# Kernel optimization log

Measured on AMD Instinct MI355X. Metric: run time of the kernel, lower is better.

Reference implementation:

```python
import jax, jax.numpy as jnp
import numpy as np

N, S, T, E, H = 4, 2048, 2048, 512, 8
HD = E // H  # head_dim = 64


def setup_inputs() -> dict:
    key0 = jax.random.key(0)
    ks = jax.random.split(key0, 12)
    sc = 1.0 / np.sqrt(E)
    inp = {
        "query": jax.random.normal(ks[0], (N, S, E), jnp.float32),
        "key": jax.random.normal(ks[1], (N, T, E), jnp.float32),
        "value": jax.random.normal(ks[2], (N, T, E), jnp.float32),
        "attn_mask": jnp.tril(jnp.ones((S, T), jnp.int32)),  # causal: 0 => masked
        # nn.Linear weights (out, in) and biases, torch convention y = x @ W.T + b
        "Wq": jax.random.normal(ks[3], (E, E), jnp.float32) * sc,
        "bq": jax.random.normal(ks[4], (E,), jnp.float32) * sc,
        "Wk": jax.random.normal(ks[5], (E, E), jnp.float32) * sc,
        "bk": jax.random.normal(ks[6], (E,), jnp.float32) * sc,
        "Wv": jax.random.normal(ks[7], (E, E), jnp.float32) * sc,
        "bv": jax.random.normal(ks[8], (E,), jnp.float32) * sc,
        "Wp": jax.random.normal(ks[9], (E, E), jnp.float32) * sc,
        "bp": jax.random.normal(ks[10], (E,), jnp.float32) * sc,
    }
    return inp


def reference(query, key, value, attn_mask, Wq, bq, Wk, bk, Wv, bv, Wp, bp):
    # QKV projections, split heads: (N, H, L, HD)
    q = (query @ Wq.T + bq).reshape(N, S, H, HD).transpose(0, 2, 1, 3)
    k = (key @ Wk.T + bk).reshape(N, T, H, HD).transpose(0, 2, 1, 3)
    v = (value @ Wv.T + bv).reshape(N, T, H, HD).transpose(0, 2, 1, 3)
    # scaled scores (N, H, S, T) -- intentionally materialized like the original
    e = jnp.einsum("nhsd,nhtd->nhst", q, k) / jnp.sqrt(jnp.float32(HD))
    e = jnp.where(attn_mask == 0, -jnp.inf, e)
    a = jax.nn.softmax(e, axis=-1)
    # dropout is identity in eval mode (reference runs deterministic/eval)
    y = jnp.einsum("nhst,nhtd->nhsd", a, v)
    y = y.transpose(0, 2, 1, 3).reshape(N, S, E)
    return y @ Wp.T + bp
```

## Files before the change

kernel.cpp:

```cpp
#include <hip/hip_runtime.h>


#define DEV __device__ __forceinline__

typedef unsigned short u16;
typedef unsigned int u32;
typedef __bf16 bf16x8 __attribute__((ext_vector_type(8)));
typedef float f32x4 __attribute__((ext_vector_type(4)));

#define MFMA_BF16(A, B, C) __builtin_amdgcn_mfma_f32_16x16x32_bf16(A, B, C, 0, 0, 0)

DEV u16 f2bf(float f) {
  u32 u = __builtin_bit_cast(u32, f);
  u += 0x7fffu + ((u >> 16) & 1u);
  return (u16)(u >> 16);
}
DEV u16 f2bf_ru(float f) {
  u32 u = __builtin_bit_cast(u32, f);
  return (u16)((u + 0x8000u) >> 16);
}

DEV void cp16(void* l, const void* g) {
  __builtin_amdgcn_global_load_lds(
      (const __attribute__((address_space(1))) u32*)g,
      (__attribute__((address_space(3))) u32*)l, 16, 0, 0);
}

__global__ __launch_bounds__(256) void cast3(const float* __restrict__ q,
                                             const float* __restrict__ k,
                                             const float* __restrict__ v,
                                             u16* qo, u16* ko, u16* vo) {
  const float* s = (blockIdx.y == 0) ? q : (blockIdx.y == 1) ? k : v;
  u16* d = (blockIdx.y == 0) ? qo : (blockIdx.y == 1) ? ko : vo;
  int i = blockIdx.x * 256 + threadIdx.x;
  float4 f = ((const float4*)s)[i];
  ushort4 o;
  o.x = f2bf(f.x); o.y = f2bf(f.y); o.z = f2bf(f.z); o.w = f2bf(f.w);
  ((ushort4*)d)[i] = o;
}

__global__ __launch_bounds__(256) void cast4(const float* __restrict__ a,
                                             const float* __restrict__ b,
                                             const float* __restrict__ c,
                                             const float* __restrict__ d2,
                                             u16* ao, u16* bo, u16* co, u16* do_) {
  int y = blockIdx.y;
  const float* s = (y == 0) ? a : (y == 1) ? b : (y == 2) ? c : d2;
  u16* d = (y == 0) ? ao : (y == 1) ? bo : (y == 2) ? co : do_;
  int i = blockIdx.x * 256 + threadIdx.x;
  float4 f = ((const float4*)s)[i];
  ushort4 o;
  o.x = f2bf(f.x); o.y = f2bf(f.y); o.z = f2bf(f.z); o.w = f2bf(f.w);
  ((ushort4*)d)[i] = o;
}

DEV void gemm_loop(const u16* __restrict__ A, const u16* __restrict__ W,
                   u16* As, u16* Bs, int m0, int n0, int tid, f32x4 acc[4][4]) {
  const int lane = tid & 63, wid = tid >> 6;
  const int wm = wid & 1, wn = wid >> 1;
  const int l15 = lane & 15, l4 = lane >> 4;
  for (int kt = 0; kt < 512; kt += 32) {
    __syncthreads();
#pragma unroll
    for (int i = 0; i < 2; ++i) {
      int c = tid + 256 * i;
      int row = c >> 2, kc = (c & 3) * 8;
      cp16(&As[c * 8], A + (m0 + row) * 512 + kt + kc);
      cp16(&Bs[c * 8], W + (n0 + row) * 512 + kt + kc);
    }
    __syncthreads();
    bf16x8 af[4], bfr[4];
#pragma unroll
    for (int f = 0; f < 4; ++f) {
      af[f]  = *(const bf16x8*)&As[(wm * 64 + f * 16 + l15) * 32 + l4 * 8];
      bfr[f] = *(const bf16x8*)&Bs[(wn * 64 + f * 16 + l15) * 32 + l4 * 8];
    }
#pragma unroll
    for (int fm = 0; fm < 4; ++fm)
#pragma unroll
      for (int fn = 0; fn < 4; ++fn)
        acc[fm][fn] = MFMA_BF16(af[fm], bfr[fn], acc[fm][fn]);
  }
}

__global__ __launch_bounds__(256) void gemm_qkv(
    const u16* __restrict__ qx, const u16* __restrict__ kx, const u16* __restrict__ vx,
    const u16* __restrict__ wq, const u16* __restrict__ wk, const u16* __restrict__ wv,
    const float* __restrict__ bq, const float* __restrict__ bk, const float* __restrict__ bv,
    u16* qp, u16* kp, u16* vp) {
  __shared__ u16 As[128 * 32];
  __shared__ u16 Bs[128 * 32];
  const int wsel = blockIdx.x >> 2;
  const u16* A = (wsel == 0) ? qx : (wsel == 1) ? kx : vx;
  const u16* W = (wsel == 0) ? wq : (wsel == 1) ? wk : wv;
  const float* bias = (wsel == 0) ? bq : (wsel == 1) ? bk : bv;
  u16* C = (wsel == 0) ? qp : (wsel == 1) ? kp : vp;
  const int n0 = (blockIdx.x & 3) * 128, m0 = blockIdx.y * 128;
  const int tid = threadIdx.x, lane = tid & 63, wid = tid >> 6;
  const int wm = wid & 1, wn = wid >> 1;
  const int l15 = lane & 15, l4 = lane >> 4;

  f32x4 acc[4][4] = {};
  gemm_loop(A, W, As, Bs, m0, n0, tid, acc);

#pragma unroll
  for (int fn = 0; fn < 4; ++fn) {
    int col = n0 + wn * 64 + fn * 16 + l15;
    float bvv = bias[col];
#pragma unroll
    for (int fm = 0; fm < 4; ++fm) {
      int rowb = m0 + wm * 64 + fm * 16 + l4 * 4;
#pragma unroll
      for (int r = 0; r < 4; ++r)
        C[(rowb + r) * 512 + col] = f2bf(acc[fm][fn][r] + bvv);
    }
  }
}

__global__ __launch_bounds__(256) void gemm_out(const u16* __restrict__ A,
                                                const u16* __restrict__ W,
                                                const float* __restrict__ bias,
                                                float* __restrict__ C) {
  __shared__ u16 As[128 * 32];
  __shared__ u16 Bs[128 * 32];
  const int n0 = blockIdx.x * 128, m0 = blockIdx.y * 128;
  const int tid = threadIdx.x, lane = tid & 63, wid = tid >> 6;
  const int wm = wid & 1, wn = wid >> 1;
  const int l15 = lane & 15, l4 = lane >> 4;

  f32x4 acc[4][4] = {};
  gemm_loop(A, W, As, Bs, m0, n0, tid, acc);

#pragma unroll
  for (int fn = 0; fn < 4; ++fn) {
    int col = n0 + wn * 64 + fn * 16 + l15;
    float bvv = bias[col];
#pragma unroll
    for (int fm = 0; fm < 4; ++fm) {
      int rowb = m0 + wm * 64 + fm * 16 + l4 * 4;
#pragma unroll
      for (int r = 0; r < 4; ++r)
        C[(rowb + r) * 512 + col] = acc[fm][fn][r] + bvv;
    }
  }
}

__global__ __launch_bounds__(256) void transpose_v(const u16* __restrict__ vp,
                                                   u16* __restrict__ vt) {
  __shared__ u16 L[64 * 72];
  const int bid = blockIdx.x;
  const int nh = bid & 31, tt = bid >> 5;
  const int n = nh >> 3, h = nh & 7;
  const u16* src = vp + (n * 2048 + tt * 64) * 512 + h * 64;
  const int tid = threadIdx.x;
#pragma unroll
  for (int i = 0; i < 2; ++i) {
    int c = tid + 256 * i;
    int row = c >> 3, dg = c & 7;
    uint4 x = *(const uint4*)(src + row * 512 + dg * 8);
    *(uint4*)&L[row * 72 + dg * 8] = x;
  }
  __syncthreads();
  u16* dst = vt + nh * 64 * 2048 + tt * 64;
#pragma unroll
  for (int i = 0; i < 2; ++i) {
    int c = tid + 256 * i;
    int d = c >> 3, tg = c & 7;
    u16 e[8];
#pragma unroll
    for (int j = 0; j < 8; ++j) e[j] = L[(tg * 8 + j) * 72 + d];
    uint4 o;
    o.x = (u32)e[0] | ((u32)e[1] << 16);
    o.y = (u32)e[2] | ((u32)e[3] << 16);
    o.z = (u32)e[4] | ((u32)e[5] << 16);
    o.w = (u32)e[6] | ((u32)e[7] << 16);
    *(uint4*)(dst + d * 2048 + tg * 8) = o;
  }
}

__global__ __launch_bounds__(256) void attn_kernel(const u16* __restrict__ Qg,
                                                   const u16* __restrict__ Kg,
                                                   const u16* __restrict__ Vt,
                                                   u16* __restrict__ Yg) {
  __shared__ u16 Qs[64 * 64];
  __shared__ u16 KP[64 * 136];
  __shared__ u16 Vts[64 * 128];

  const int bid = blockIdx.x;
  const int nh = bid & 31;
  const int qt = 31 - (bid >> 5);
  const int n = nh >> 3, h = nh & 7;
  const int tid = threadIdx.x, lane = tid & 63, w = tid >> 6;
  const int l15 = lane & 15, l4 = lane >> 4;
  const int s0 = qt * 64;

  const u16* Qb = Qg + (n * 2048 + s0) * 512 + h * 64;
  const u16* Kb = Kg + n * 2048 * 512 + h * 64;
  const u16* Vb = Vt + nh * 64 * 2048;

#pragma unroll
  for (int i = 0; i < 2; ++i) {
    int c = tid + 256 * i;
    int row = c >> 3, dg = (c & 7) ^ (row & 7);
    cp16(&Qs[c * 8], Qb + row * 512 + dg * 8);
  }
  __syncthreads();
  const int qr = w * 16 + l15;
  bf16x8 qf0 = *(const bf16x8*)&Qs[qr * 64 + ((l4 ^ (qr & 7)) * 8)];
  bf16x8 qf1 = *(const bf16x8*)&Qs[qr * 64 + (((4 + l4) ^ (qr & 7)) * 8)];

  f32x4 accO[4] = {};
  float mrow = -1e30f, lrow = 0.f;
  const int sgl = s0 + w * 16 + l15;

  const int ntiles = (qt >> 1) + 1;
  for (int it = 0; it < ntiles; ++it) {
    const int t0 = it * 128;
    __syncthreads();
#pragma unroll
    for (int i = 0; i < 4; ++i) {
      int c = tid + 256 * i;
      int t = c >> 3, dg = (c & 7) ^ (t & 7);
      cp16(&KP[c * 8], Kb + (t0 + t) * 512 + dg * 8);
    }
#pragma unroll
    for (int i = 0; i < 4; ++i) {
      int c = tid + 256 * i;
      int d = c >> 4, tgs = c & 15;
      cp16(&Vts[c * 8], Vb + d * 2048 + t0 + ((tgs ^ (d & 15)) * 8));
    }
    __syncthreads();

    f32x4 st[8];
#pragma unroll
    for (int fn = 0; fn < 8; ++fn) {
      int tr = fn * 16 + l15;
      bf16x8 k0 = *(const bf16x8*)&KP[tr * 64 + ((l4 ^ (tr & 7)) * 8)];
      bf16x8 k1 = *(const bf16x8*)&KP[tr * 64 + (((4 + l4) ^ (tr & 7)) * 8)];
      f32x4 a = {};
      a = MFMA_BF16(k0, qf0, a);
      st[fn] = MFMA_BF16(k1, qf1, a);
    }

    const bool diag = (t0 + 128 > s0);
    const float SC = 0.18033688f;
    float rmax = -1e30f;
#pragma unroll
    for (int fn = 0; fn < 8; ++fn)
#pragma unroll
      for (int r = 0; r < 4; ++r) {
        float v = st[fn][r] * SC;
        if (diag) {
          int tg = t0 + fn * 16 + l4 * 4 + r;
          if (tg > sgl) v = -1e30f;
        }
        st[fn][r] = v;
        rmax = fmaxf(rmax, v);
      }
    rmax = fmaxf(rmax, __shfl_xor(rmax, 16));
    rmax = fmaxf(rmax, __shfl_xor(rmax, 32));
    float mnew = fmaxf(mrow, rmax);
    float alpha = __builtin_amdgcn_exp2f(mrow - mnew);
    mrow = mnew;
    float rsum = 0.f;
#pragma unroll
    for (int fn = 0; fn < 8; ++fn)
#pragma unroll
      for (int r = 0; r < 4; ++r) {
        float p = __builtin_amdgcn_exp2f(st[fn][r] - mnew);
        st[fn][r] = p;
        rsum += p;
      }
    rsum += __shfl_xor(rsum, 16);
    rsum += __shfl_xor(rsum, 32);
    lrow = lrow * alpha + rsum;

    float aO[4];
#pragma unroll
    for (int r = 0; r < 4; ++r) aO[r] = __shfl(alpha, (lane & 48) | (l4 * 4 + r));
#pragma unroll
    for (int fd = 0; fd < 4; ++fd)
#pragma unroll
      for (int r = 0; r < 4; ++r) accO[fd][r] *= aO[r];

    __syncthreads();

#pragma unroll
    for (int fn = 0; fn < 8; ++fn) {
      ushort4 pk;
      pk.x = f2bf_ru(st[fn][0]);
      pk.y = f2bf_ru(st[fn][1]);
      pk.z = f2bf_ru(st[fn][2]);
      pk.w = f2bf_ru(st[fn][3]);
      *(ushort4*)&KP[(w * 16 + l15) * 136 + fn * 16 + l4 * 4] = pk;
    }

#pragma unroll
    for (int ks = 0; ks < 4; ++ks) {
      bf16x8 ap = *(const bf16x8*)&KP[(w * 16 + l15) * 136 + ks * 32 + l4 * 8];
#pragma unroll
      for (int fd = 0; fd < 4; ++fd) {
        int d = fd * 16 + l15;
        bf16x8 bv = *(const bf16x8*)&Vts[d * 128 + (((ks * 4 + l4) ^ (d & 15)) * 8)];
        accO[fd] = MFMA_BF16(ap, bv, accO[fd]);
      }
    }
  }

  float lO[4];
#pragma unroll
  for (int r = 0; r < 4; ++r) lO[r] = __shfl(lrow, (lane & 48) | (l4 * 4 + r));
#pragma unroll
  for (int fd = 0; fd < 4; ++fd)
#pragma unroll
    for (int r = 0; r < 4; ++r) {
      int row = s0 + w * 16 + l4 * 4 + r;
      int col = h * 64 + fd * 16 + l15;
      Yg[(n * 2048 + row) * 512 + col] = f2bf(accO[fd][r] / lO[r]);
    }
}

extern "C" void kernel_launch(void* const* d_in, const int* in_sizes, int n_in,
                              void* d_out, int out_size, void* d_ws, size_t ws_size,
                              hipStream_t stream) {
  (void)in_sizes; (void)n_in; (void)out_size; (void)ws_size;
  const float* query = (const float*)d_in[0];
  const float* key_  = (const float*)d_in[1];
  const float* value = (const float*)d_in[2];
  const float* Wq = (const float*)d_in[4];
  const float* bq = (const float*)d_in[5];
  const float* Wk = (const float*)d_in[6];
  const float* bk = (const float*)d_in[7];
  const float* Wv = (const float*)d_in[8];
  const float* bv = (const float*)d_in[9];
  const float* Wp = (const float*)d_in[10];
  const float* bp = (const float*)d_in[11];

  char* ws = (char*)d_ws;
  u16* qx  = (u16*)(ws);
  u16* kx  = (u16*)(ws + 8388608);
  u16* vx  = (u16*)(ws + 16777216);
  u16* wqx = (u16*)(ws + 25165824);
  u16* wkx = (u16*)(ws + 25690112);
  u16* wvx = (u16*)(ws + 26214400);
  u16* wpx = (u16*)(ws + 26738688);
  u16* qp  = (u16*)(ws + 27262976);
  u16* kp  = (u16*)(ws + 35651584);
  u16* vp  = (u16*)(ws + 44040192);
  u16* y   = qx;
  u16* vt  = kx;

  cast3<<<dim3(4096, 3), 256, 0, stream>>>(query, key_, value, qx, kx, vx);
  cast4<<<dim3(256, 4), 256, 0, stream>>>(Wq, Wk, Wv, Wp, wqx, wkx, wvx, wpx);

  gemm_qkv<<<dim3(12, 64), 256, 0, stream>>>(qx, kx, vx, wqx, wkx, wvx,
                                             bq, bk, bv, qp, kp, vp);
  transpose_v<<<1024, 256, 0, stream>>>(vp, vt);
  attn_kernel<<<1024, 256, 0, stream>>>(qp, kp, vt, y);
  gemm_out<<<dim3(4, 64), 256, 0, stream>>>(y, wpx, bp, (float*)d_out);
}
```

Baseline: 209.5 us.

## Rework attention to 32x32 MFMA 128-row tiles, fuse V transpose and casts

The two cast kernels are merged into one launch, and the softmax scale is folded into Wq and bq during the cast. The V transpose kernel is removed: the QKV GEMM epilogue now writes V directly in transposed per-head layout. The attention kernel is rewritten to handle 128-query tiles with 32x32x16 MFMAs, skip fully masked key fragments on the diagonal tile, and use a reorganised swizzled LDS layout for P. Halving the block count and making tiles larger cuts launch and reload overhead, but raises LDS use and register pressure. The balanced qt ordering is also changed.

```diff
diff --git a/kernel.cpp b/kernel.cpp
--- a/kernel.cpp
+++ b/kernel.cpp
@@ -7,8 +7,12 @@
 typedef unsigned int u32;
 typedef __bf16 bf16x8 __attribute__((ext_vector_type(8)));
 typedef float f32x4 __attribute__((ext_vector_type(4)));
-
-#define MFMA_BF16(A, B, C) __builtin_amdgcn_mfma_f32_16x16x32_bf16(A, B, C, 0, 0, 0)
+typedef float f32x16 __attribute__((ext_vector_type(16)));
+
+#define MFMA16(A, B, C) __builtin_amdgcn_mfma_f32_16x16x32_bf16(A, B, C, 0, 0, 0)
+#define MFMA32(A, B, C) __builtin_amdgcn_mfma_f32_32x32x16_bf16(A, B, C, 0, 0, 0)
+
+#define SC 0.18033688f
 
 DEV u16 f2bf(float f) {
   u32 u = __builtin_bit_cast(u32, f);
@@ -26,31 +30,32 @@
       (__attribute__((address_space(3))) u32*)l, 16, 0, 0);
 }
 
-__global__ __launch_bounds__(256) void cast3(const float* __restrict__ q,
-                                             const float* __restrict__ k,
-                                             const float* __restrict__ v,
-                                             u16* qo, u16* ko, u16* vo) {
-  const float* s = (blockIdx.y == 0) ? q : (blockIdx.y == 1) ? k : v;
-  u16* d = (blockIdx.y == 0) ? qo : (blockIdx.y == 1) ? ko : vo;
-  int i = blockIdx.x * 256 + threadIdx.x;
+__global__ __launch_bounds__(256) void cast_all(
+    const float* __restrict__ q, const float* __restrict__ k, const float* __restrict__ v,
+    const float* __restrict__ wq, const float* __restrict__ wk, const float* __restrict__ wv,
+    const float* __restrict__ wp,
+    u16* qo, u16* ko, u16* vo, u16* wqo, u16* wko, u16* wvo, u16* wpo) {
+  int b = blockIdx.x, tid = threadIdx.x;
+  const float* s;
+  u16* d;
+  int off;
+  float sc = 1.f;
+  if (b < 12288) {
+    int which = b >> 12;
+    s = (which == 0) ? q : (which == 1) ? k : v;
+    d = (which == 0) ? qo : (which == 1) ? ko : vo;
+    off = (b & 4095) * 256;
+  } else {
+    int wb = b - 12288, which = wb >> 8;
+    s = (which == 0) ? wq : (which == 1) ? wk : (which == 2) ? wv : wp;
+    d = (which == 0) ? wqo : (which == 1) ? wko : (which == 2) ? wvo : wpo;
+    off = (wb & 255) * 256;
+    if (which == 0) sc = SC;
+  }
+  int i = off + tid;
   float4 f = ((const float4*)s)[i];
   ushort4 o;
-  o.x = f2bf(f.x); o.y = f2bf(f.y); o.z = f2bf(f.z); o.w = f2bf(f.w);
-  ((ushort4*)d)[i] = o;
-}
-
-__global__ __launch_bounds__(256) void cast4(const float* __restrict__ a,
-                                             const float* __restrict__ b,
-                                             const float* __restrict__ c,
-                                             const float* __restrict__ d2,
-                                             u16* ao, u16* bo, u16* co, u16* do_) {
-  int y = blockIdx.y;
-  const float* s = (y == 0) ? a : (y == 1) ? b : (y == 2) ? c : d2;
-  u16* d = (y == 0) ? ao : (y == 1) ? bo : (y == 2) ? co : do_;
-  int i = blockIdx.x * 256 + threadIdx.x;
-  float4 f = ((const float4*)s)[i];
-  ushort4 o;
-  o.x = f2bf(f.x); o.y = f2bf(f.y); o.z = f2bf(f.z); o.w = f2bf(f.w);
+  o.x = f2bf(f.x * sc); o.y = f2bf(f.y * sc); o.z = f2bf(f.z * sc); o.w = f2bf(f.w * sc);
   ((ushort4*)d)[i] = o;
 }
 
@@ -79,7 +84,7 @@
     for (int fm = 0; fm < 4; ++fm)
 #pragma unroll
       for (int fn = 0; fn < 4; ++fn)
-        acc[fm][fn] = MFMA_BF16(af[fm], bfr[fn], acc[fm][fn]);
+        acc[fm][fn] = MFMA16(af[fm], bfr[fn], acc[fm][fn]);
   }
 }
 
@@ -87,14 +92,13 @@
     const u16* __restrict__ qx, const u16* __restrict__ kx, const u16* __restrict__ vx,
     const u16* __restrict__ wq, const u16* __restrict__ wk, const u16* __restrict__ wv,
     const float* __restrict__ bq, const float* __restrict__ bk, const float* __restrict__ bv,
-    u16* qp, u16* kp, u16* vp) {
+    u16* qp, u16* kp, u16* vt) {
   __shared__ u16 As[128 * 32];
   __shared__ u16 Bs[128 * 32];
   const int wsel = blockIdx.x >> 2;
   const u16* A = (wsel == 0) ? qx : (wsel == 1) ? kx : vx;
   const u16* W = (wsel == 0) ? wq : (wsel == 1) ? wk : wv;
   const float* bias = (wsel == 0) ? bq : (wsel == 1) ? bk : bv;
-  u16* C = (wsel == 0) ? qp : (wsel == 1) ? kp : vp;
   const int n0 = (blockIdx.x & 3) * 128, m0 = blockIdx.y * 128;
   const int tid = threadIdx.x, lane = tid & 63, wid = tid >> 6;
   const int wm = wid & 1, wn = wid >> 1;
@@ -103,16 +107,38 @@
   f32x4 acc[4][4] = {};
   gemm_loop(A, W, As, Bs, m0, n0, tid, acc);
 
-#pragma unroll
-  for (int fn = 0; fn < 4; ++fn) {
-    int col = n0 + wn * 64 + fn * 16 + l15;
-    float bvv = bias[col];
-#pragma unroll
-    for (int fm = 0; fm < 4; ++fm) {
-      int rowb = m0 + wm * 64 + fm * 16 + l4 * 4;
-#pragma unroll
-      for (int r = 0; r < 4; ++r)
-        C[(rowb + r) * 512 + col] = f2bf(acc[fm][fn][r] + bvv);
+  if (wsel < 2) {
+    u16* C = (wsel == 0) ? qp : kp;
+    const float bscale = (wsel == 0) ? SC : 1.f;
+#pragma unroll
+    for (int fn = 0; fn < 4; ++fn) {
+      int col = n0 + wn * 64 + fn * 16 + l15;
+      float bvv = bias[col] * bscale;
+#pragma unroll
+      for (int fm = 0; fm < 4; ++fm) {
+        int rowb = m0 + wm * 64 + fm * 16 + l4 * 4;
+#pragma unroll
+        for (int r = 0; r < 4; ++r)
+          C[(rowb + r) * 512 + col] = f2bf(acc[fm][fn][r] + bvv);
+      }
+    }
+  } else {
+    const int nIdx = m0 >> 11, tb = m0 & 2047;
+#pragma unroll
+    for (int fn = 0; fn < 4; ++fn) {
+      int col = n0 + wn * 64 + fn * 16 + l15;
+      int vtrow = (nIdx * 8 + (col >> 6)) * 64 + (col & 63);
+      float bvv = bias[col];
+#pragma unroll
+      for (int fm = 0; fm < 4; ++fm) {
+        int t = tb + wm * 64 + fm * 16 + l4 * 4;
+        ushort4 o;
+        o.x = f2bf(acc[fm][fn][0] + bvv);
+        o.y = f2bf(acc[fm][fn][1] + bvv);
+        o.z = f2bf(acc[fm][fn][2] + bvv);
+        o.w = f2bf(acc[fm][fn][3] + bvv);
+        *(ushort4*)(vt + vtrow * 2048 + t) = o;
+      }
     }
   }
 }
@@ -145,178 +171,155 @@
   }
 }
 
-__global__ __launch_bounds__(256) void transpose_v(const u16* __restrict__ vp,
-                                                   u16* __restrict__ vt) {
-  __shared__ u16 L[64 * 72];
-  const int bid = blockIdx.x;
-  const int nh = bid & 31, tt = bid >> 5;
-  const int n = nh >> 3, h = nh & 7;
-  const u16* src = vp + (n * 2048 + tt * 64) * 512 + h * 64;
-  const int tid = threadIdx.x;
-#pragma unroll
-  for (int i = 0; i < 2; ++i) {
-    int c = tid + 256 * i;
-    int row = c >> 3, dg = c & 7;
-    uint4 x = *(const uint4*)(src + row * 512 + dg * 8);
-    *(uint4*)&L[row * 72 + dg * 8] = x;
-  }
-  __syncthreads();
-  u16* dst = vt + nh * 64 * 2048 + tt * 64;
-#pragma unroll
-  for (int i = 0; i < 2; ++i) {
-    int c = tid + 256 * i;
-    int d = c >> 3, tg = c & 7;
-    u16 e[8];
-#pragma unroll
-    for (int j = 0; j < 8; ++j) e[j] = L[(tg * 8 + j) * 72 + d];
-    uint4 o;
-    o.x = (u32)e[0] | ((u32)e[1] << 16);
-    o.y = (u32)e[2] | ((u32)e[3] << 16);
-    o.z = (u32)e[4] | ((u32)e[5] << 16);
-    o.w = (u32)e[6] | ((u32)e[7] << 16);
-    *(uint4*)(dst + d * 2048 + tg * 8) = o;
-  }
-}
-
 __global__ __launch_bounds__(256) void attn_kernel(const u16* __restrict__ Qg,
                                                    const u16* __restrict__ Kg,
                                                    const u16* __restrict__ Vt,
                                                    u16* __restrict__ Yg) {
-  __shared__ u16 Qs[64 * 64];
-  __shared__ u16 KP[64 * 136];
-  __shared__ u16 Vts[64 * 128];
+  __shared__ u16 Ps[128 * 128];
+  __shared__ u16 Ks[128 * 64];
+  __shared__ u16 Vs[64 * 128];
 
   const int bid = blockIdx.x;
   const int nh = bid & 31;
-  const int qt = 31 - (bid >> 5);
+  const int p = bid >> 5;
+  const int qt = (p < 8) ? (15 - p) : (p - 8);
   const int n = nh >> 3, h = nh & 7;
   const int tid = threadIdx.x, lane = tid & 63, w = tid >> 6;
-  const int l15 = lane & 15, l4 = lane >> 4;
-  const int s0 = qt * 64;
+  const int l31 = lane & 31, lh = lane >> 5;
+  const int s0 = qt * 128;
 
   const u16* Qb = Qg + (n * 2048 + s0) * 512 + h * 64;
   const u16* Kb = Kg + n * 2048 * 512 + h * 64;
   const u16* Vb = Vt + nh * 64 * 2048;
 
 #pragma unroll
-  for (int i = 0; i < 2; ++i) {
-    int c = tid + 256 * i;
-    int row = c >> 3, dg = (c & 7) ^ (row & 7);
-    cp16(&Qs[c * 8], Qb + row * 512 + dg * 8);
+  for (int i = 0; i < 4; ++i) {
+    int ci = tid + 256 * i;
+    int m = ci >> 3, pc = ci & 7;
+    cp16(&Ps[ci * 8], Qb + m * 512 + ((pc ^ (m & 7)) * 8));
   }
   __syncthreads();
-  const int qr = w * 16 + l15;
-  bf16x8 qf0 = *(const bf16x8*)&Qs[qr * 64 + ((l4 ^ (qr & 7)) * 8)];
-  bf16x8 qf1 = *(const bf16x8*)&Qs[qr * 64 + (((4 + l4) ^ (qr & 7)) * 8)];
-
-  f32x4 accO[4] = {};
+  const int qm = w * 32 + l31;
+  bf16x8 qf[4];
+#pragma unroll
+  for (int ks = 0; ks < 4; ++ks)
+    qf[ks] = *(const bf16x8*)&Ps[qm * 64 + (((2 * ks + lh) ^ (qm & 7)) * 8)];
+
+  f32x16 accO[2] = {};
   float mrow = -1e30f, lrow = 0.f;
-  const int sgl = s0 + w * 16 + l15;
-
-  const int ntiles = (qt >> 1) + 1;
-  for (int it = 0; it < ntiles; ++it) {
+
+  for (int it = 0; it <= qt; ++it) {
     const int t0 = it * 128;
     __syncthreads();
 #pragma unroll
     for (int i = 0; i < 4; ++i) {
-      int c = tid + 256 * i;
-      int t = c >> 3, dg = (c & 7) ^ (t & 7);
-      cp16(&KP[c * 8], Kb + (t0 + t) * 512 + dg * 8);
+      int ci = tid + 256 * i;
+      int t = ci >> 3, pc = ci & 7;
+      cp16(&Ks[ci * 8], Kb + (t0 + t) * 512 + ((pc ^ (t & 7)) * 8));
     }
 #pragma unroll
     for (int i = 0; i < 4; ++i) {
-      int c = tid + 256 * i;
-      int d = c >> 4, tgs = c & 15;
-      cp16(&Vts[c * 8], Vb + d * 2048 + t0 + ((tgs ^ (d & 15)) * 8));
+      int ci = tid + 256 * i;
+      int d = ci >> 4, pc = ci & 15;
+      cp16(&Vs[ci * 8], Vb + d * 2048 + t0 + ((pc ^ (d & 15)) * 8));
     }
     __syncthreads();
 
-    f32x4 st[8];
-#pragma unroll
-    for (int fn = 0; fn < 8; ++fn) {
-      int tr = fn * 16 + l15;
-      bf16x8 k0 = *(const bf16x8*)&KP[tr * 64 + ((l4 ^ (tr & 7)) * 8)];
-      bf16x8 k1 = *(const bf16x8*)&KP[tr * 64 + (((4 + l4) ^ (tr & 7)) * 8)];
-      f32x4 a = {};
-      a = MFMA_BF16(k0, qf0, a);
-      st[fn] = MFMA_BF16(k1, qf1, a);
-    }
-
-    const bool diag = (t0 + 128 > s0);
-    const float SC = 0.18033688f;
+    const bool diag = (it == qt);
+    const int nf = diag ? (w + 1) : 4;
+
+    f32x16 st[4];
+#pragma unroll
+    for (int f = 0; f < 4; ++f)
+      if (f < nf) {
+        f32x16 a = {};
+        int tr = f * 32 + l31;
+#pragma unroll
+        for (int ks = 0; ks < 4; ++ks) {
+          bf16x8 kf = *(const bf16x8*)&Ks[tr * 64 + (((2 * ks + lh) ^ (tr & 7)) * 8)];
+          a = MFMA32(kf, qf[ks], a);
+        }
+        if (diag && f == w) {
+#pragma unroll
+          for (int r = 0; r < 16; ++r) {
+            int trow = f * 32 + (r & 3) + 8 * (r >> 2) + 4 * lh;
+            a[r] = (trow > qm) ? -1e30f : a[r];
+          }
+        }
+        st[f] = a;
+      }
+
     float rmax = -1e30f;
 #pragma unroll
-    for (int fn = 0; fn < 8; ++fn)
-#pragma unroll
-      for (int r = 0; r < 4; ++r) {
-        float v = st[fn][r] * SC;
-        if (diag) {
-          int tg = t0 + fn * 16 + l4 * 4 + r;
-          if (tg > sgl) v = -1e30f;
-        }
-        st[fn][r] = v;
-        rmax = fmaxf(rmax, v);
-      }
-    rmax = fmaxf(rmax, __shfl_xor(rmax, 16));
+    for (int f = 0; f < 4; ++f)
+      if (f < nf)
+#pragma unroll
+        for (int r = 0; r < 16; ++r) rmax = fmaxf(rmax, st[f][r]);
     rmax = fmaxf(rmax, __shfl_xor(rmax, 32));
     float mnew = fmaxf(mrow, rmax);
     float alpha = __builtin_amdgcn_exp2f(mrow - mnew);
     mrow = mnew;
     float rsum = 0.f;
 #pragma unroll
-    for (int fn = 0; fn < 8; ++fn)
-#pragma unroll
-      for (int r = 0; r < 4; ++r) {
-        float p = __builtin_amdgcn_exp2f(st[fn][r] - mnew);
-        st[fn][r] = p;
-        rsum += p;
-      }
-    rsum += __shfl_xor(rsum, 16);
+    for (int f = 0; f < 4; ++f)
+      if (f < nf)
+#pragma unroll
+        for (int r = 0; r < 16; ++r) {
+          float pv = __builtin_amdgcn_exp2f(st[f][r] - mnew);
+          st[f][r] = pv;
+          rsum += pv;
+        }
     rsum += __shfl_xor(rsum, 32);
     lrow = lrow * alpha + rsum;
-
-    float aO[4];
-#pragma unroll
-    for (int r = 0; r < 4; ++r) aO[r] = __shfl(alpha, (lane & 48) | (l4 * 4 + r));
-#pragma unroll
-    for (int fd = 0; fd < 4; ++fd)
-#pragma unroll
-      for (int r = 0; r < 4; ++r) accO[fd][r] *= aO[r];
-
-    __syncthreads();
-
-#pragma unroll
-    for (int fn = 0; fn < 8; ++fn) {
-      ushort4 pk;
-      pk.x = f2bf_ru(st[fn][0]);
-      pk.y = f2bf_ru(st[fn][1]);
-      pk.z = f2bf_ru(st[fn][2]);
-      pk.w = f2bf_ru(st[fn][3]);
-      *(ushort4*)&KP[(w * 16 + l15) * 136 + fn * 16 + l4 * 4] = pk;
-    }
-
-#pragma unroll
-    for (int ks = 0; ks < 4; ++ks) {
-      bf16x8 ap = *(const bf16x8*)&KP[(w * 16 + l15) * 136 + ks * 32 + l4 * 8];
-#pragma unroll
-      for (int fd = 0; fd < 4; ++fd) {
-        int d = fd * 16 + l15;
-        bf16x8 bv = *(const bf16x8*)&Vts[d * 128 + (((ks * 4 + l4) ^ (d & 15)) * 8)];
-        accO[fd] = MFMA_BF16(ap, bv, accO[fd]);
+    accO[0] = accO[0] * alpha;
+    accO[1] = accO[1] * alpha;
+
+    const int pbase = qm * 128;
+#pragma unroll
+    for (int f = 0; f < 4; ++f)
+      if (f < nf)
+#pragma unroll
+        for (int g = 0; g < 4; ++g) {
+          ushort4 pk;
+          pk.x = f2bf_ru(st[f][4 * g + 0]);
+          pk.y = f2bf_ru(st[f][4 * g + 1]);
+          pk.z = f2bf_ru(st[f][4 * g + 2]);
+          pk.w = f2bf_ru(st[f][4 * g + 3]);
+          int c8 = f * 8 + 2 * g + lh;
+          *(ushort4*)&Ps[pbase + ((c8 ^ (qm & 31)) * 4)] = pk;
+        }
+
+    const int nks = nf * 2;
+#pragma unroll
+    for (int ks = 0; ks < 8; ++ks)
+      if (ks < nks) {
+        int c8a = 4 * ks + 2 * lh;
+        uint2 lo = *(const uint2*)&Ps[pbase + ((c8a ^ (qm & 31)) * 4)];
+        uint2 hi = *(const uint2*)&Ps[pbase + (((c8a + 1) ^ (qm & 31)) * 4)];
+        uint4 pb4;
+        pb4.x = lo.x; pb4.y = lo.y; pb4.z = hi.x; pb4.w = hi.y;
+        bf16x8 pb = __builtin_bit_cast(bf16x8, pb4);
+#pragma unroll
+        for (int fd = 0; fd < 2; ++fd) {
+          int d = fd * 32 + l31;
+          bf16x8 vf = *(const bf16x8*)&Vs[d * 128 + (((2 * ks + lh) ^ (d & 15)) * 8)];
+          accO[fd] = MFMA32(vf, pb, accO[fd]);
+        }
       }
-    }
-  }
-
-  float lO[4];
-#pragma unroll
-  for (int r = 0; r < 4; ++r) lO[r] = __shfl(lrow, (lane & 48) | (l4 * 4 + r));
-#pragma unroll
-  for (int fd = 0; fd < 4; ++fd)
-#pragma unroll
-    for (int r = 0; r < 4; ++r) {
-      int row = s0 + w * 16 + l4 * 4 + r;
-      int col = h * 64 + fd * 16 + l15;
-      Yg[(n * 2048 + row) * 512 + col] = f2bf(accO[fd][r] / lO[r]);
+  }
+
+  float inv = 1.0f / lrow;
+  u16* Yb = Yg + (n * 2048 + s0 + qm) * 512 + h * 64;
+#pragma unroll
+  for (int fd = 0; fd < 2; ++fd)
+#pragma unroll
+    for (int g = 0; g < 4; ++g) {
+      ushort4 o;
+      o.x = f2bf(accO[fd][4 * g + 0] * inv);
+      o.y = f2bf(accO[fd][4 * g + 1] * inv);
+      o.z = f2bf(accO[fd][4 * g + 2] * inv);
+      o.w = f2bf(accO[fd][4 * g + 3] * inv);
+      *(ushort4*)(Yb + fd * 32 + 8 * g + 4 * lh) = o;
     }
 }
 
@@ -346,16 +349,13 @@
   u16* wpx = (u16*)(ws + 26738688);
   u16* qp  = (u16*)(ws + 27262976);
   u16* kp  = (u16*)(ws + 35651584);
-  u16* vp  = (u16*)(ws + 44040192);
+  u16* vt  = (u16*)(ws + 44040192);
   u16* y   = qx;
-  u16* vt  = kx;
-
-  cast3<<<dim3(4096, 3), 256, 0, stream>>>(query, key_, value, qx, kx, vx);
-  cast4<<<dim3(256, 4), 256, 0, stream>>>(Wq, Wk, Wv, Wp, wqx, wkx, wvx, wpx);
-
+
+  cast_all<<<13312, 256, 0, stream>>>(query, key_, value, Wq, Wk, Wv, Wp,
+                                      qx, kx, vx, wqx, wkx, wvx, wpx);
   gemm_qkv<<<dim3(12, 64), 256, 0, stream>>>(qx, kx, vx, wqx, wkx, wvx,
-                                             bq, bk, bv, qp, kp, vp);
-  transpose_v<<<1024, 256, 0, stream>>>(vp, vt);
-  attn_kernel<<<1024, 256, 0, stream>>>(qp, kp, vt, y);
+                                             bq, bk, bv, qp, kp, vt);
+  attn_kernel<<<512, 256, 0, stream>>>(qp, kp, vt, y);
   gemm_out<<<dim3(4, 64), 256, 0, stream>>>(y, wpx, bp, (float*)d_out);
 }
```

Measured after the change: 225.6 us. 7.7% more time.
